# Optimization experiments

Hardware: AMD Instinct MI355X
Metric: run time of the kernel (lower is better)

Reference implementation:

```python
import jax, jax.numpy as jnp
import numpy as np

B, S, C = 16, 1024, 8
V, D, E, H, R = 50257, 512, 8, 512, 32
F, RT, CD, Q = 1024, 512, 64, 128
EPS = 1e-6


def _normalize(x):
    n = jnp.maximum(jnp.linalg.norm(x, axis=-1, keepdims=True), EPS)
    return x / n


def _fake_quantize(x):
    # F.normalize then straight-through int8 quant on the unit vector
    xn = _normalize(x)
    q = jnp.clip(jnp.round(xn * 127.0), -127.0, 127.0)
    return xn + jax.lax.stop_gradient(q / 127.0 - xn)


def setup_inputs() -> dict:
    key = jax.random.key(0)
    ks = iter(jax.random.split(key, 64))

    def w(shape, s=0.02):
        return (jax.random.normal(next(ks), shape, dtype=jnp.float32) * s)

    inp = {}
    inp['prefix_tokens'] = jax.random.randint(next(ks), (B, S), 0, V, dtype=jnp.int32)
    inp['chunk_inputs'] = jax.random.randint(next(ks), (B, C), 0, V, dtype=jnp.int32)
    inp['chunk_targets'] = jax.random.randint(next(ks), (B, C), 0, V, dtype=jnp.int32)
    inp['next_chunk_tokens'] = jax.random.randint(next(ks), (B, C), 0, V, dtype=jnp.int32)

    inp['emb'] = w((V, D))
    # stacked per-expert AffineExpert params
    inp['Wa'] = w((E, D, H)); inp['ba'] = jnp.zeros((E, H), jnp.float32)
    inp['Wg'] = w((E, D, R)); inp['bg'] = jnp.zeros((E, R), jnp.float32)
    inp['Wu'] = w((E, D, H)); inp['bu'] = jnp.zeros((E, H), jnp.float32)
    inp['u_mat'] = w((E, H, R)); inp['v_mat'] = w((E, H, R))
    inp['Wp'] = w((E, H, F)); inp['bp'] = jnp.zeros((E, F), jnp.float32)
    # gate MLP
    inp['Wg1'] = w((D, D)); inp['bg1'] = jnp.zeros((D,), jnp.float32)
    inp['Wg2'] = w((D, E)); inp['bg2'] = jnp.zeros((E,), jnp.float32)
    # query / target / key / code-expansion / write-code
    inp['Wq'] = w((F, Q)); inp['bq'] = jnp.zeros((Q,), jnp.float32)
    inp['Wt1'] = w((2 * D, RT)); inp['bt1'] = jnp.zeros((RT,), jnp.float32)
    inp['Wt2'] = w((RT, RT)); inp['bt2'] = jnp.zeros((RT,), jnp.float32)
    inp['Wk'] = w((RT, Q)); inp['bk'] = jnp.zeros((Q,), jnp.float32)
    inp['Web'] = w((CD, RT))  # expansion_basis (no bias)
    inp['Wwc'] = w((F, CD)); inp['bwc'] = jnp.zeros((CD,), jnp.float32)
    # ctx MLP
    inp['Wc1'] = w((2 * F, F)); inp['bc1'] = jnp.zeros((F,), jnp.float32)
    inp['Wc2'] = w((F, F)); inp['bc2'] = jnp.zeros((F,), jnp.float32)
    # chunk decoder
    inp['chunk_pos'] = w((C, F))
    inp['Wci'] = w((D + F, F)); inp['bci'] = jnp.zeros((F,), jnp.float32)
    inp['Wm1'] = w((F, F)); inp['bm1'] = jnp.zeros((F,), jnp.float32)
    inp['Wm2'] = w((F, F)); inp['bm2'] = jnp.zeros((F,), jnp.float32)
    inp['Wlm'] = w((F, V)); inp['blm'] = jnp.zeros((V,), jnp.float32)
    return inp


def _expert_scan(x, Wa, ba, Wg, bg, Wu, bu, u_mat, v_mat):
    # x: [B,S,D]; precompute all per-step projections as one big GEMM each,
    # leading axis = time for lax.scan. A,U: [S,E,B,H], G: [S,E,B,R]
    A = jax.nn.sigmoid(jnp.einsum('bsd,edh->sebh', x, Wa) + ba[None, :, None, :])
    G = jnp.einsum('bsd,edr->sebr', x, Wg) + bg[None, :, None, :]
    U = jnp.einsum('bsd,edh->sebh', x, Wu) + bu[None, :, None, :]

    def step(state, inp):  # state: [E,B,H]
        a, g, u = inp
        low = jnp.einsum('ebh,ehr->ebr', state, v_mat) * g
        state = a * state + u + jnp.einsum('ebr,ehr->ebh', low, u_mat)
        return state, None

    state0 = jnp.zeros((E, B, H), x.dtype)
    state, _ = jax.lax.scan(step, state0, (A, G, U))
    return state  # [E,B,H]


def reference(prefix_tokens, chunk_inputs, chunk_targets, next_chunk_tokens,
              emb, Wa, ba, Wg, bg, Wu, bu, u_mat, v_mat, Wp, bp,
              Wg1, bg1, Wg2, bg2, Wq, bq, Wt1, bt1, Wt2, bt2, Wk, bk,
              Web, Wwc, bwc, Wc1, bc1, Wc2, bc2,
              chunk_pos, Wci, bci, Wm1, bm1, Wm2, bm2, Wlm, blm):
    # ---- encode_prefix ----
    prefix_emb = emb[prefix_tokens]                       # [B,S,D]
    summary = prefix_emb.mean(axis=1)                     # [B,D]
    gate_probs = jax.nn.softmax(jax.nn.silu(summary @ Wg1 + bg1) @ Wg2 + bg2, axis=-1)  # [B,E]
    states = _expert_scan(prefix_emb, Wa, ba, Wg, bg, Wu, bu, u_mat, v_mat)             # [E,B,H]
    proj = jnp.einsum('ebh,ehf->ebf', states, Wp) + bp[:, None, :]                       # [E,B,F]
    fused = jnp.einsum('ebf,be->bf', proj, gate_probs)    # [B,F]

    # ---- query / target / key ----
    q_st = _fake_quantize(fused @ Wq + bq)                # [B,Q]
    chunk_emb = emb[chunk_targets].mean(axis=1)           # [B,D]
    next_emb = emb[next_chunk_tokens].mean(axis=1)        # [B,D]
    t_in = jnp.concatenate([chunk_emb, next_emb], axis=-1)
    target_state = _normalize(jax.nn.silu(t_in @ Wt1 + bt1) @ Wt2 + bt2)  # [B,RT]
    target_k_st = _fake_quantize(target_state @ Wk + bk)  # [B,Q]

    # ---- read_context (bank=None path -> zero read) ----
    zero_read = jnp.zeros_like(fused)
    c_in = jnp.concatenate([fused, zero_read], axis=-1)
    ctx = jax.nn.silu(c_in @ Wc1 + bc1) @ Wc2 + bc2       # [B,F]

    # ---- write_from_ctx ----
    write_codes = ctx @ Wwc + bwc                         # [B,CD]
    write_state = _normalize(write_codes @ Web)           # [B,RT]
    write_k_st = _fake_quantize(write_state @ Wk + bk)    # [B,Q]

    # ---- decode_chunk ----
    tok = emb[chunk_inputs]                               # [B,C,D]
    ctx_rep = jnp.broadcast_to(ctx[:, None, :], (B, C, F))
    hidden = jnp.concatenate([tok, ctx_rep], axis=-1) @ Wci + bci + chunk_pos[None]  # [B,C,F]
    hidden = jax.nn.silu(hidden @ Wm1 + bm1) @ Wm2 + bm2
    logits = hidden @ Wlm + blm                           # [B,C,V]

    # ---- losses ----
    logp = jax.nn.log_softmax(logits, axis=-1)
    token_loss = -jnp.take_along_axis(logp, chunk_targets[..., None], axis=-1)[..., 0]
    loss_nll = token_loss.mean()
    sim = (q_st @ target_k_st.T) / jnp.sqrt(jnp.float32(Q))  # [B,B]
    return logits, loss_nll, sim, write_k_st
```

## Files before the change

### kernel.cpp

```cpp
#include <hip/hip_runtime.h>
#include <math.h>

constexpr int BB = 16;
constexpr int SS = 1024;
constexpr int CC = 8;
constexpr int VV = 50257;
constexpr int DD = 512;
constexpr int EE = 8;
constexpr int HH = 512;
constexpr int RR = 32;
constexpr int FF = 1024;
constexpr int RTd = 512;
constexpr int CDd = 64;
constexpr int QQ = 128;
constexpr int SCH = 128;

typedef short bf16x8 __attribute__((ext_vector_type(8)));
typedef float f32x4 __attribute__((ext_vector_type(4)));

__device__ __forceinline__ float sigm(float x){ return 1.0f/(1.0f+expf(-x)); }

__device__ __forceinline__ unsigned short f2bf(float f){
  unsigned int u = __float_as_uint(f);
  u += 0x7fff + ((u>>16)&1);
  return (unsigned short)(u>>16);
}
__device__ __forceinline__ float bf2f(unsigned short h){
  return __uint_as_float(((unsigned int)h)<<16);
}

__device__ __forceinline__ void gload16(unsigned short* l, const unsigned short* g){
  __builtin_amdgcn_global_load_lds(
      (const __attribute__((address_space(1))) unsigned int*)(g),
      (__attribute__((address_space(3))) unsigned int*)(l), 16, 0, 0);
}

__global__ __launch_bounds__(256) void gather_pack(const int* __restrict__ toks,
    const float* __restrict__ emb, unsigned short* __restrict__ xp){
  int id = blockIdx.x*256 + threadIdx.x;
  int b = id >> 17;
  int rem = id & 131071;
  int c = rem >> 14;
  int rem2 = rem & 16383;
  int kc = rem2 >> 10;
  int pb = rem2 & 1023;
  int row = pb >> 3, q = pb & 7;
  int v = q ^ (row & 7);
  int kq = v >> 1, h = v & 1;
  int tok = toks[b*SS + c*128 + row];
  const float* src = emb + (size_t)tok*DD + kc*32 + kq*8;
  unsigned short o[8];
  #pragma unroll
  for (int j=0;j<8;j++){
    float f = src[j];
    unsigned short hi = f2bf(f);
    o[j] = h ? f2bf(f - bf2f(hi)) : hi;
  }
  ushort4* dst = (ushort4*)(xp + (size_t)id*8);
  dst[0] = make_ushort4(o[0],o[1],o[2],o[3]);
  dst[1] = make_ushort4(o[4],o[5],o[6],o[7]);
}

__global__ __launch_bounds__(512) void colsum_part(const int* __restrict__ toks,
    const float* __restrict__ emb, float* __restrict__ part){
  int b = blockIdx.y, j = blockIdx.x, d = threadIdx.x;
  float s = 0.f;
  for (int k=0;k<64;k++){
    int tok = toks[b*SS + j*64 + k];
    s += emb[(size_t)tok*DD + d];
  }
  part[(b*16 + j)*DD + d] = s;
}
__global__ __launch_bounds__(512) void colsum_final(const float* __restrict__ part,
                                                    float* __restrict__ summary){
  int b = blockIdx.x, d = threadIdx.x;
  float s = 0.f;
  for (int j=0;j<16;j++) s += part[(b*16 + j)*DD + d];
  summary[b*DD + d] = s * (1.0f/1024.0f);
}

__global__ __launch_bounds__(128) void gate_h1(const float* __restrict__ summary,
                                               const float* __restrict__ Wg1,
                                               const float* __restrict__ bg1,
                                               float* __restrict__ h1){
  int t = threadIdx.x; int j = blockIdx.x*128 + t;
  __shared__ float sm[16*512];
  for (int idx=t; idx<8192; idx+=128) sm[idx] = summary[idx];
  __syncthreads();
  float acc[16] = {0};
  for (int d=0; d<DD; d++){
    float w = Wg1[d*DD + j];
    #pragma unroll
    for (int b2=0;b2<16;b2++) acc[b2] += sm[b2*DD + d]*w;
  }
  #pragma unroll
  for (int b2=0;b2<16;b2++){ float v = acc[b2] + bg1[j]; h1[b2*DD + j] = v*sigm(v); }
}
__global__ __launch_bounds__(128) void gate_probs_k(const float* __restrict__ h1,
                                                    const float* __restrict__ Wg2,
                                                    const float* __restrict__ bg2,
                                                    float* __restrict__ gate){
  int t = threadIdx.x;
  int b = t>>3, e = t&7;
  float acc = bg2[e];
  for (int d=0; d<DD; d++) acc += h1[b*DD + d]*Wg2[d*EE + e];
  __shared__ float lg[16][8];
  lg[b][e] = acc;
  __syncthreads();
  if (e==0){
    float m = -3.4e38f;
    for (int i=0;i<8;i++) m = fmaxf(m, lg[b][i]);
    float s = 0.f; float ex[8];
    for (int i=0;i<8;i++){ ex[i] = expf(lg[b][i]-m); s += ex[i]; }
    for (int i=0;i<8;i++) gate[b*EE + i] = ex[i]/s;
  }
}

__global__ __launch_bounds__(256) void convT_pack_au(const float* __restrict__ Wa,
    const float* __restrict__ Wu, unsigned short* __restrict__ WPackAU){
  const int bid = blockIdx.x;
  const int e = bid >> 5;
  const int au = (bid >> 4) & 1;
  const int kc = bid & 15;
  const float* W = (au ? Wu : Wa) + (size_t)e*DD*HH + (size_t)kc*32*HH;
  __shared__ float tw[32][513];
  const int t = threadIdx.x;
  for (int i=0;i<64;i++){
    int id = t + i*256;
    int c = id & 511, k = id >> 9;
    tw[k][c] = W[(size_t)k*HH + c];
  }
  __syncthreads();
  for (int i=0;i<16;i++){
    int slot = t + i*256;
    int wq = slot >> 10, rem = slot & 1023;
    int cf = rem >> 7, hl = (rem >> 6) & 1, lane = rem & 63;
    int col = wq*128 + cf*16 + (lane & 15);
    int kb = lane >> 4;
    unsigned short o[8];
    #pragma unroll
    for (int j=0;j<8;j++){
      float f = tw[kb*8 + j][col];
      unsigned short hi = f2bf(f);
      o[j] = hl ? f2bf(f - bf2f(hi)) : hi;
    }
    size_t dst = (size_t)(e*2+au)*524288 + (size_t)(wq*16 + kc)*8192
               + (size_t)(cf*2 + hl)*512 + lane*8;
    *(ushort4*)&WPackAU[dst]   = make_ushort4(o[0],o[1],o[2],o[3]);
    *(ushort4*)&WPackAU[dst+4] = make_ushort4(o[4],o[5],o[6],o[7]);
  }
}
__global__ __launch_bounds__(256) void convT_pack_g(const float* __restrict__ Wge,
    unsigned short* __restrict__ WPG){
  const int kc = blockIdx.x;
  __shared__ float tg[32][257];
  const int t = threadIdx.x;
  for (int i=0;i<32;i++){
    int id = t + i*256;
    int r = id & 31, k = (id >> 5) & 31, e = id >> 10;
    tg[k][e*32 + r] = Wge[((size_t)e*DD + kc*32 + k)*RR + r];
  }
  __syncthreads();
  for (int i=0;i<8;i++){
    int slot = t + i*256;
    int w = slot >> 8, rem = slot & 255;
    int cf = rem >> 7, hl = (rem >> 6) & 1, lane = rem & 63;
    int gcol = w*32 + cf*16 + (lane & 15);
    int kb = lane >> 4;
    unsigned short o[8];
    #pragma unroll
    for (int j=0;j<8;j++){
      float f = tg[kb*8 + j][gcol];
      unsigned short hi = f2bf(f);
      o[j] = hl ? f2bf(f - bf2f(hi)) : hi;
    }
    size_t dst = (((size_t)(w*16 + kc)*2 + cf)*2 + hl)*512 + lane*8;
    *(ushort4*)&WPG[dst]   = make_ushort4(o[0],o[1],o[2],o[3]);
    *(ushort4*)&WPG[dst+4] = make_ushort4(o[4],o[5],o[6],o[7]);
  }
}

__global__ __launch_bounds__(512, 2) void aug_scan(
    const unsigned short* __restrict__ xp,
    const unsigned short* __restrict__ WPackAU, const unsigned short* __restrict__ WPG,
    const float* __restrict__ ba, const float* __restrict__ bu, const float* __restrict__ bge,
    float* __restrict__ Aw, float* __restrict__ Uw, float* __restrict__ Gw,
    const float* __restrict__ Ar, const float* __restrict__ Ur, const float* __restrict__ Gr,
    const float* __restrict__ v_mat, const float* __restrict__ u_mat,
    float* __restrict__ states,
    int s0, int do_aug, int do_scan)
{
  __shared__ __align__(16) unsigned short lds[65536];
  const int t = threadIdx.x;
  const int xcd  = blockIdx.x & 7;
  const int slot = blockIdx.x >> 3;

  if (slot < 16){
    if (!do_scan) return;
    const int e = xcd;
    const int b = slot;
    const int r = t & 31, grp = t >> 5;
    float* stf   = (float*)lds;
    float* partf = (float*)lds + 1024;
    float* lowf  = (float*)lds + 1312;
    float vreg[32];
    #pragma unroll
    for (int i=0;i<32;i++) vreg[i] = v_mat[((size_t)e*HH + grp*32 + i)*RR + r];
    float ureg[32];
    {
      const float4* up = (const float4*)(u_mat + ((size_t)e*HH + t)*RR);
      #pragma unroll
      for (int j=0;j<8;j++){
        float4 v4 = up[j];
        ureg[j*4+0]=v4.x; ureg[j*4+1]=v4.y; ureg[j*4+2]=v4.z; ureg[j*4+3]=v4.w;
      }
    }
    const size_t sbase = ((size_t)e*BB + b)*HH + t;
    const size_t abase = ((size_t)e*BB + b)*SCH*HH + t;
    const size_t gbase = ((size_t)e*BB + b)*SCH*RR + r;
    float streg = states[sbase];
    stf[t] = streg;
    float a0 = Ar[abase], u0 = Ur[abase];
    float g0 = (t < 32) ? Gr[gbase] : 0.f;
    float a1 = Ar[abase + HH], u1 = Ur[abase + HH];
    float g1 = (t < 32) ? Gr[gbase + RR] : 0.f;
    __syncthreads();
    int cur = 0;
    for (int s=0; s<SCH; s++){
      float a2 = 0.f, u2 = 0.f, g2 = 0.f;
      if (s+2 < SCH){
        a2 = Ar[abase + (size_t)(s+2)*HH];
        u2 = Ur[abase + (size_t)(s+2)*HH];
        if (t < 32) g2 = Gr[gbase + (size_t)(s+2)*RR];
      }
      {
        const float* sp = &stf[cur*512 + grp*32];
        float p0=0.f,p1=0.f,p2=0.f,p3=0.f;
        #pragma unroll
        for (int i=0;i<8;i++){
          p0 += sp[i]    *vreg[i];
          p1 += sp[8+i]  *vreg[8+i];
          p2 += sp[16+i] *vreg[16+i];
          p3 += sp[24+i] *vreg[24+i];
        }
        float p = (p0+p1)+(p2+p3);
        p += __shfl_xor(p, 32, 64);
        if ((t & 32) == 0) partf[r*9 + (grp>>1)] = p;
      }
      __syncthreads();
      if (t < 32){
        float ss2 = 0.f;
        #pragma unroll
        for (int j=0;j<8;j++) ss2 += partf[t*9 + j];
        lowf[t] = ss2 * g0;
      }
      __syncthreads();
      {
        float q0=0.f,q1=0.f,q2=0.f,q3=0.f;
        #pragma unroll
        for (int i=0;i<8;i++){
          q0 += lowf[i]   *ureg[i];
          q1 += lowf[8+i] *ureg[8+i];
          q2 += lowf[16+i]*ureg[16+i];
          q3 += lowf[24+i]*ureg[24+i];
        }
        streg = a0*streg + u0 + ((q0+q1)+(q2+q3));
      }
      stf[(cur^1)*512 + t] = streg;
      cur ^= 1;
      a0=a1; u0=u1; g0=g1; a1=a2; u1=u2; g1=g2;
      __syncthreads();
    }
    states[sbase] = streg;
    return;
  }

  if (!do_aug) return;
  const int lane = t & 63, wv = t >> 6;
  const int cl15 = lane & 15;
  const int kb = lane >> 4;
  const int cix = s0 >> 7;

  if (slot < 48){
    const int e = xcd;
    const int idx = slot - 16;
    const int b = idx & 15;
    const int r0 = (idx >> 4) * 64;
    const unsigned short* xpc = xp + (((size_t)(b*8 + cix)) << 17);
    const int au = wv >> 2, wq = wv & 3;
    const unsigned short* wb = WPackAU + (size_t)(e*2+au)*524288 + (size_t)wq*16*8192;

    {
      const int kc = wv;
      const unsigned short* src = xpc + kc*8192 + r0*64;
      unsigned short* dst = lds + kc*4096;
      #pragma unroll
      for (int i=0;i<8;i++)
        gload16(dst + i*512, src + (size_t)(i*64 + lane)*8);
    }
    __syncthreads();
    {
      const int kc = 8 + wv;
      const unsigned short* src = xpc + kc*8192 + r0*64;
      unsigned short* dst = lds + kc*4096;
      #pragma unroll
      for (int i=0;i<8;i++)
        gload16(dst + i*512, src + (size_t)(i*64 + lane)*8);
    }

    f32x4 acc[4][8] = {};
    for (int half=0; half<2; half++){
      if (half) __syncthreads();
      for (int kc = half*8; kc < half*8 + 8; kc++){
        bf16x8 ah[4], al[4];
        #pragma unroll
        for (int rf=0; rf<4; rf++){
          const int rloc = rf*16 + cl15;
          const int qh = (kb*2) ^ (rloc & 7);
          ah[rf] = *(const bf16x8*)&lds[kc*4096 + rloc*64 + qh*8];
          al[rf] = *(const bf16x8*)&lds[kc*4096 + rloc*64 + (qh^1)*8];
        }
        #pragma unroll
        for (int cf=0; cf<8; cf++){
          const unsigned short* fp = wb + ((size_t)kc*8 + cf)*1024 + lane*8;
          bf16x8 bh = *(const bf16x8*)fp;
          bf16x8 bl = *(const bf16x8*)(fp + 512);
          #pragma unroll
          for (int rf=0; rf<4; rf++){
            acc[rf][cf] = __builtin_amdgcn_mfma_f32_16x16x32_bf16(ah[rf], bh, acc[rf][cf], 0,0,0);
            acc[rf][cf] = __builtin_amdgcn_mfma_f32_16x16x32_bf16(ah[rf], bl, acc[rf][cf], 0,0,0);
            acc[rf][cf] = __builtin_amdgcn_mfma_f32_16x16x32_bf16(al[rf], bh, acc[rf][cf], 0,0,0);
          }
        }
      }
    }
    const float* bias = au ? bu : ba;
    float* dst = (au ? Uw : Aw) + ((size_t)(e*BB + b)*SCH + r0)*HH;
    #pragma unroll
    for (int rf=0; rf<4; rf++){
      #pragma unroll
      for (int cf=0; cf<8; cf++){
        const int col = wq*128 + cf*16 + cl15;
        const float bv = bias[e*HH + col];
        #pragma unroll
        for (int i=0;i<4;i++){
          const int rloc = rf*16 + (lane>>4)*4 + i;
          float v = acc[rf][cf][i] + bv;
          if (!au) v = sigm(v);
          dst[(size_t)rloc*HH + col] = v;
        }
      }
    }
  } else {
    const int idx2 = slot - 48;
    const int b = (xcd << 1) | (idx2 & 1);
    const int r0 = (idx2 >> 1) * 32;
    const unsigned short* xpc = xp + (((size_t)(b*8 + cix)) << 17);
    {
      const int kc = wv;
      const unsigned short* src = xpc + kc*8192 + r0*64;
      unsigned short* dst = lds + kc*2048;
      #pragma unroll
      for (int i=0;i<4;i++)
        gload16(dst + i*512, src + (size_t)(i*64 + lane)*8);
    }
    __syncthreads();
    {
      const int kc = 8 + wv;
      const unsigned short* src = xpc + kc*8192 + r0*64;
      unsigned short* dst = lds + kc*2048;
      #pragma unroll
      for (int i=0;i<4;i++)
        gload16(dst + i*512, src + (size_t)(i*64 + lane)*8);
    }
    f32x4 acc[2][2] = {};
    const unsigned short* wb = WPG + (size_t)wv*32768;
    for (int half=0; half<2; half++){
      if (half) __syncthreads();
      for (int kc = half*8; kc < half*8 + 8; kc++){
        bf16x8 ah[2], al[2];
        #pragma unroll
        for (int rf=0; rf<2; rf++){
          const int rloc = rf*16 + cl15;
          const int qh = (kb*2) ^ (rloc & 7);
          ah[rf] = *(const bf16x8*)&lds[kc*2048 + rloc*64 + qh*8];
          al[rf] = *(const bf16x8*)&lds[kc*2048 + rloc*64 + (qh^1)*8];
        }
        #pragma unroll
        for (int cf=0; cf<2; cf++){
          const unsigned short* fp = wb + ((size_t)kc*2 + cf)*1024 + lane*8;
          bf16x8 bh = *(const bf16x8*)fp;
          bf16x8 bl = *(const bf16x8*)(fp + 512);
          #pragma unroll
          for (int rf=0; rf<2; rf++){
            acc[rf][cf] = __builtin_amdgcn_mfma_f32_16x16x32_bf16(ah[rf], bh, acc[rf][cf], 0,0,0);
            acc[rf][cf] = __builtin_amdgcn_mfma_f32_16x16x32_bf16(ah[rf], bl, acc[rf][cf], 0,0,0);
            acc[rf][cf] = __builtin_amdgcn_mfma_f32_16x16x32_bf16(al[rf], bh, acc[rf][cf], 0,0,0);
          }
        }
      }
    }
    #pragma unroll
    for (int rf=0; rf<2; rf++){
      #pragma unroll
      for (int cf=0; cf<2; cf++){
        const int gcol = wv*32 + cf*16 + cl15;
        const int ee = gcol >> 5, r = gcol & 31;
        const float bv = bge[ee*RR + r];
        #pragma unroll
        for (int i=0;i<4;i++){
          const int rloc = rf*16 + (lane>>4)*4 + i;
          Gw[((size_t)(ee*BB + b)*SCH + r0 + rloc)*RR + r] = acc[rf][cf][i] + bv;
        }
      }
    }
  }
}

__global__ __launch_bounds__(128) void proj_partial(const float* __restrict__ states,
    const float* __restrict__ Wp, const float* __restrict__ gate, float* __restrict__ pf){
  int fc = blockIdx.x, e = blockIdx.y, t = threadIdx.x;
  __shared__ float stl[16*512];
  for (int idx=t; idx<8192; idx+=128) stl[idx] = states[(size_t)e*8192 + idx];
  __syncthreads();
  int f = fc*128 + t;
  float acc[16] = {0};
  for (int h=0; h<HH; h++){
    float w = Wp[((size_t)e*HH + h)*FF + f];
    #pragma unroll
    for (int b2=0;b2<16;b2++) acc[b2] += stl[b2*HH + h]*w;
  }
  #pragma unroll
  for (int b2=0;b2<16;b2++) pf[((size_t)(e*16 + b2))*FF + f] = gate[b2*EE + e]*acc[b2];
}
__global__ __launch_bounds__(256) void fuse_reduce(const float* __restrict__ pf,
    const float* __restrict__ gate, const float* __restrict__ bp, float* __restrict__ fused){
  int idx = blockIdx.x*256 + threadIdx.x;
  int b = idx >> 10, f = idx & 1023;
  float s = 0.f;
  #pragma unroll
  for (int e=0;e<8;e++) s += pf[((size_t)(e*16 + b))*FF + f] + gate[b*EE + e]*bp[e*FF + f];
  fused[idx] = s;
}

__global__ __launch_bounds__(128) void fq_linear(const float* __restrict__ in, int Kin,
    const float* __restrict__ W, const float* __restrict__ bias, float* __restrict__ out){
  int b = blockIdx.x, t = threadIdx.x;
  __shared__ float xin[1024];
  __shared__ float red[2];
  for (int k=t;k<Kin;k+=128) xin[k] = in[(size_t)b*Kin + k];
  __syncthreads();
  float acc = bias[t];
  for (int k=0;k<Kin;k++) acc += xin[k]*W[k*QQ + t];
  float ss = acc*acc;
  #pragma unroll
  for (int off=32; off; off>>=1) ss += __shfl_xor(ss, off, 64);
  if ((t&63)==0) red[t>>6] = ss;
  __syncthreads();
  float n = fmaxf(sqrtf(red[0]+red[1]), 1e-6f);
  float xn = acc / n;
  float q = fminf(fmaxf(rintf(xn*127.0f), -127.0f), 127.0f) * (1.0f/127.0f);
  out[b*QQ + t] = q;
}

__global__ __launch_bounds__(512) void chunk_means(const int* __restrict__ ct,
    const int* __restrict__ nct, const float* __restrict__ emb, float* __restrict__ tin){
  int b = blockIdx.x, d = threadIdx.x;
  float ce=0.f, ne=0.f;
  for (int c=0;c<CC;c++){
    ce += emb[(size_t)ct[b*CC+c]*DD + d];
    ne += emb[(size_t)nct[b*CC+c]*DD + d];
  }
  tin[b*1024 + d] = ce*0.125f;
  tin[b*1024 + 512 + d] = ne*0.125f;
}

__global__ __launch_bounds__(512) void target_state_kernel(const float* __restrict__ tin,
    const float* __restrict__ Wt1, const float* __restrict__ bt1,
    const float* __restrict__ Wt2, const float* __restrict__ bt2, float* __restrict__ outts){
  int b = blockIdx.x, t = threadIdx.x;
  __shared__ float xin[1024];
  __shared__ float h1[512];
  __shared__ float red[8];
  for (int k=t;k<1024;k+=512) xin[k] = tin[b*1024 + k];
  __syncthreads();
  float acc = bt1[t];
  for (int k=0;k<1024;k++) acc += xin[k]*Wt1[k*RTd + t];
  acc = acc*sigm(acc);
  h1[t] = acc;
  __syncthreads();
  float y = bt2[t];
  for (int k=0;k<512;k++) y += h1[k]*Wt2[k*RTd + t];
  float ss = y*y;
  #pragma unroll
  for (int off=32; off; off>>=1) ss += __shfl_xor(ss, off, 64);
  if ((t&63)==0) red[t>>6] = ss;
  __syncthreads();
  float tot = 0.f;
  #pragma unroll
  for (int i=0;i<8;i++) tot += red[i];
  float n = fmaxf(sqrtf(tot), 1e-6f);
  outts[b*RTd + t] = y/n;
}

__global__ __launch_bounds__(512) void write_state_kernel(const float* __restrict__ ctx,
    const float* __restrict__ Wwc, const float* __restrict__ bwc,
    const float* __restrict__ Web, float* __restrict__ wsn){
  int b = blockIdx.x, t = threadIdx.x;
  __shared__ float cx[1024];
  __shared__ float wc[64];
  __shared__ float red[8];
  for (int k=t;k<1024;k+=512) cx[k] = ctx[b*FF + k];
  __syncthreads();
  if (t < 64){
    float a = bwc[t];
    for (int k=0;k<1024;k++) a += cx[k]*Wwc[k*CDd + t];
    wc[t] = a;
  }
  __syncthreads();
  float y = 0.f;
  for (int k=0;k<64;k++) y += wc[k]*Web[k*RTd + t];
  float ss = y*y;
  #pragma unroll
  for (int off=32; off; off>>=1) ss += __shfl_xor(ss, off, 64);
  if ((t&63)==0) red[t>>6] = ss;
  __syncthreads();
  float tot = 0.f;
  #pragma unroll
  for (int i=0;i<8;i++) tot += red[i];
  float n = fmaxf(sqrtf(tot), 1e-6f);
  wsn[b*RTd + t] = y/n;
}

__global__ __launch_bounds__(256) void sim_kernel(const float* __restrict__ q,
    const float* __restrict__ k, float* __restrict__ out){
  int t = threadIdx.x;
  int i = t>>4, j = t&15;
  float s = 0.f;
  for (int c=0;c<QQ;c++) s += q[i*QQ + c]*k[j*QQ + c];
  out[t] = s / sqrtf(128.0f);
}

__global__ __launch_bounds__(256) void build_xcat(const int* __restrict__ ci,
    const float* __restrict__ emb, const float* __restrict__ ctx, float* __restrict__ xcat){
  int idx = blockIdx.x*256 + threadIdx.x;
  int row = idx / 1536, k = idx % 1536;
  float v = (k < DD) ? emb[(size_t)ci[row]*DD + k] : ctx[(row>>3)*FF + (k - DD)];
  xcat[idx] = v;
}

__global__ __launch_bounds__(256) void gemm_part(const float* __restrict__ X,
    const float* __restrict__ W, float* __restrict__ part,
    int K, int KS, int M){
  const int t = threadIdx.x;
  const int col = blockIdx.x*64 + (t & 63);
  const int r0 = blockIdx.y*16;
  const int ks = blockIdx.z;
  const int rg = t >> 6;
  const int kslice = K / KS;
  const int kbeg = ks*kslice;
  __shared__ float xs[16][65];
  float acc[4] = {};
  for (int k0=kbeg; k0<kbeg+kslice; k0+=64){
    #pragma unroll
    for (int i=0;i<4;i++){
      int id = t + i*256;
      int row = id >> 6, kk = id & 63;
      xs[row][kk] = X[(size_t)(r0+row)*K + k0 + kk];
    }
    __syncthreads();
    #pragma unroll 8
    for (int kk=0; kk<64; kk++){
      float w = W[(size_t)(k0+kk)*FF + col];
      #pragma unroll
      for (int i=0;i<4;i++) acc[i] += xs[rg*4+i][kk]*w;
    }
    __syncthreads();
  }
  #pragma unroll
  for (int i=0;i<4;i++)
    part[((size_t)ks*M + r0 + rg*4 + i)*FF + col] = acc[i];
}
__global__ __launch_bounds__(256) void gemm_combine(const float* __restrict__ part,
    const float* __restrict__ bias, const float* __restrict__ pos,
    float* __restrict__ outp, int KS, int M, int act){
  int idx = blockIdx.x*256 + threadIdx.x;
  int row = idx >> 10, col = idx & 1023;
  float v = bias[col];
  for (int k=0;k<KS;k++) v += part[(size_t)k*M*FF + idx];
  if (pos) v += pos[(row & 7)*FF + col];
  if (act) v = v*sigm(v);
  outp[idx] = v;
}

__global__ __launch_bounds__(256) void split_h(const float* __restrict__ hsrc,
    unsigned short* __restrict__ hh, unsigned short* __restrict__ hl){
  int idx = blockIdx.x*256 + threadIdx.x;
  float f = hsrc[idx];
  unsigned short h = f2bf(f);
  hh[idx] = h;
  hl[idx] = f2bf(f - bf2f(h));
}

__global__ __launch_bounds__(256) void logits_mfma(
    const unsigned short* __restrict__ hh, const unsigned short* __restrict__ hl,
    const float* __restrict__ Wlm, const float* __restrict__ blm,
    float* __restrict__ out){
  const int t = threadIdx.x;
  const int lane = t & 63, w = t >> 6;
  const int cb = blockIdx.x * 64;
  __shared__ __align__(16) unsigned short xsh[8*128*8];
  __shared__ __align__(16) unsigned short xsl[8*128*8];
  __shared__ __align__(16) unsigned short wsh[8*64*8];
  __shared__ __align__(16) unsigned short wsl[8*64*8];
  f32x4 acc[2][4] = {};
  for (int kc=0; kc<16; kc++){
    const int k0 = kc*64;
    #pragma unroll
    for (int i=0;i<4;i++){
      int id = t + i*256;
      int kq = id & 7, row = id >> 3;
      int pb = row*8 + (kq ^ (row&7));
      *(uint4*)&xsh[pb*8] = *(const uint4*)(hh + (size_t)row*FF + k0 + kq*8);
      *(uint4*)&xsl[pb*8] = *(const uint4*)(hl + (size_t)row*FF + k0 + kq*8);
    }
    #pragma unroll
    for (int i=0;i<2;i++){
      int id = t + i*256;
      int cc = id & 63, kq = id >> 6;
      int c = cb + cc; if (c >= VV) c = VV - 1;
      unsigned short h8[8], l8[8];
      #pragma unroll
      for (int j=0;j<8;j++){
        float f = Wlm[(size_t)(k0 + kq*8 + j)*VV + c];
        unsigned short h = f2bf(f);
        h8[j] = h;
        l8[j] = f2bf(f - bf2f(h));
      }
      int pb = kq*64 + cc;
      *(ushort4*)&wsh[pb*8]   = make_ushort4(h8[0],h8[1],h8[2],h8[3]);
      *(ushort4*)&wsh[pb*8+4] = make_ushort4(h8[4],h8[5],h8[6],h8[7]);
      *(ushort4*)&wsl[pb*8]   = make_ushort4(l8[0],l8[1],l8[2],l8[3]);
      *(ushort4*)&wsl[pb*8+4] = make_ushort4(l8[4],l8[5],l8[6],l8[7]);
    }
    __syncthreads();
    #pragma unroll
    for (int ks=0; ks<2; ks++){
      const int kq4 = ks*4 + (lane>>4);
      const int rr0 = w*32 + (lane&15);
      const int rr1 = rr0 + 16;
      bf16x8 ah0 = *(const bf16x8*)&xsh[(rr0*8 + (kq4^(rr0&7)))*8];
      bf16x8 ah1 = *(const bf16x8*)&xsh[(rr1*8 + (kq4^(rr1&7)))*8];
      bf16x8 al0 = *(const bf16x8*)&xsl[(rr0*8 + (kq4^(rr0&7)))*8];
      bf16x8 al1 = *(const bf16x8*)&xsl[(rr1*8 + (kq4^(rr1&7)))*8];
      #pragma unroll
      for (int cf=0; cf<4; cf++){
        const int cc = cf*16 + (lane&15);
        bf16x8 bh = *(const bf16x8*)&wsh[(kq4*64 + cc)*8];
        bf16x8 bl = *(const bf16x8*)&wsl[(kq4*64 + cc)*8];
        acc[0][cf] = __builtin_amdgcn_mfma_f32_16x16x32_bf16(ah0, bh, acc[0][cf], 0,0,0);
        acc[0][cf] = __builtin_amdgcn_mfma_f32_16x16x32_bf16(ah0, bl, acc[0][cf], 0,0,0);
        acc[0][cf] = __builtin_amdgcn_mfma_f32_16x16x32_bf16(al0, bh, acc[0][cf], 0,0,0);
        acc[1][cf] = __builtin_amdgcn_mfma_f32_16x16x32_bf16(ah1, bh, acc[1][cf], 0,0,0);
        acc[1][cf] = __builtin_amdgcn_mfma_f32_16x16x32_bf16(ah1, bl, acc[1][cf], 0,0,0);
        acc[1][cf] = __builtin_amdgcn_mfma_f32_16x16x32_bf16(al1, bh, acc[1][cf], 0,0,0);
      }
    }
    __syncthreads();
  }
  const int cl = lane & 15;
  const int r4 = (lane >> 4) * 4;
  #pragma unroll
  for (int rf=0; rf<2; rf++){
    #pragma unroll
    for (int cf=0; cf<4; cf++){
      int c = cb + cf*16 + cl;
      if (c >= VV) continue;
      float bb = blm[c];
      #pragma unroll
      for (int i=0;i<4;i++){
        int row = w*32 + rf*16 + r4 + i;
        out[(size_t)row*VV + c] = acc[rf][cf][i] + bb;
      }
    }
  }
}

__global__ __launch_bounds__(512) void softmax_nll(const float* __restrict__ logits,
    const int* __restrict__ tgt, float* __restrict__ tl){
  const int row = blockIdx.x;
  const float* p = logits + (size_t)row*VV;
  const int t = threadIdx.x;
  float m = -3.4e38f, s = 0.f;
  for (int c=t; c<VV; c+=512){
    float v = p[c];
    if (v > m){ s = s*expf(m - v) + 1.0f; m = v; }
    else s += expf(v - m);
  }
  #pragma unroll
  for (int off=32; off; off>>=1){
    float m2 = __shfl_xor(m, off, 64);
    float s2 = __shfl_xor(s, off, 64);
    float mn = fmaxf(m, m2);
    s = s*expf(m - mn) + s2*expf(m2 - mn);
    m = mn;
  }
  __shared__ float ms[8], ssh[8];
  if ((t&63)==0){ ms[t>>6] = m; ssh[t>>6] = s; }
  __syncthreads();
  if (t==0){
    float M = ms[0], S = ssh[0];
    for (int i=1;i<8;i++){
      float mn = fmaxf(M, ms[i]);
      S = S*expf(M-mn) + ssh[i]*expf(ms[i]-mn);
      M = mn;
    }
    tl[row] = M + logf(S) - p[tgt[row]];
  }
}
__global__ __launch_bounds__(128) void loss_reduce(const float* __restrict__ tl,
                                                   float* __restrict__ out){
  int t = threadIdx.x;
  float v = tl[t];
  #pragma unroll
  for (int off=32; off; off>>=1) v += __shfl_xor(v, off, 64);
  __shared__ float r2[2];
  if ((t&63)==0) r2[t>>6] = v;
  __syncthreads();
  if (t==0) out[0] = (r2[0]+r2[1]) * (1.0f/128.0f);
}

extern "C" void kernel_launch(void* const* d_in, const int* in_sizes, int n_in,
                              void* d_out, int out_size, void* d_ws, size_t ws_size,
                              hipStream_t stream){
  (void)in_sizes; (void)n_in; (void)out_size;
  const int*  prefix = (const int*)d_in[0];
  const int*  cinp   = (const int*)d_in[1];
  const int*  ctgt   = (const int*)d_in[2];
  const int*  nctk   = (const int*)d_in[3];
  const float* emb  = (const float*)d_in[4];
  const float* Wa   = (const float*)d_in[5];
  const float* ba   = (const float*)d_in[6];
  const float* Wge  = (const float*)d_in[7];
  const float* bge  = (const float*)d_in[8];
  const float* Wu   = (const float*)d_in[9];
  const float* bu   = (const float*)d_in[10];
  const float* u_mat= (const float*)d_in[11];
  const float* v_mat= (const float*)d_in[12];
  const float* Wp   = (const float*)d_in[13];
  const float* bp   = (const float*)d_in[14];
  const float* Wg1  = (const float*)d_in[15];
  const float* bg1  = (const float*)d_in[16];
  const float* Wg2  = (const float*)d_in[17];
  const float* bg2  = (const float*)d_in[18];
  const float* Wq   = (const float*)d_in[19];
  const float* bq   = (const float*)d_in[20];
  const float* Wt1  = (const float*)d_in[21];
  const float* bt1  = (const float*)d_in[22];
  const float* Wt2  = (const float*)d_in[23];
  const float* bt2  = (const float*)d_in[24];
  const float* Wk   = (const float*)d_in[25];
  const float* bk   = (const float*)d_in[26];
  const float* Web  = (const float*)d_in[27];
  const float* Wwc  = (const float*)d_in[28];
  const float* bwc  = (const float*)d_in[29];
  const float* Wc1  = (const float*)d_in[30];
  const float* bc1  = (const float*)d_in[31];
  const float* Wc2  = (const float*)d_in[32];
  const float* bc2  = (const float*)d_in[33];
  const float* cpos = (const float*)d_in[34];
  const float* Wci  = (const float*)d_in[35];
  const float* bci  = (const float*)d_in[36];
  const float* Wm1  = (const float*)d_in[37];
  const float* bm1  = (const float*)d_in[38];
  const float* Wm2  = (const float*)d_in[39];
  const float* bm2  = (const float*)d_in[40];
  const float* Wlm  = (const float*)d_in[41];
  const float* blm  = (const float*)d_in[42];

  float* ws = (float*)d_ws;
  size_t off = 0;
  unsigned short* xp = (unsigned short*)(ws + off); off += (size_t)BB*SS*DD;
  float* Abuf0  = ws + off; off += (size_t)SCH*EE*BB*HH;
  float* Ubuf0  = ws + off; off += (size_t)SCH*EE*BB*HH;
  float* Gbuf0  = ws + off; off += (size_t)SCH*EE*BB*RR;
  float* statesb= ws + off; off += (size_t)EE*BB*HH;
  float* partb  = ws + off; off += (size_t)BB*16*DD;
  float* summb  = ws + off; off += (size_t)BB*DD;
  float* h1b    = ws + off; off += (size_t)BB*DD;
  float* gateb  = ws + off; off += (size_t)BB*EE;
  float* pfb    = ws + off; off += (size_t)EE*BB*FF;
  float* fusedb = ws + off; off += (size_t)BB*FF;
  float* qstb   = ws + off; off += (size_t)BB*QQ;
  float* tinb   = ws + off; off += (size_t)BB*2*DD;
  float* tstb   = ws + off; off += (size_t)BB*RTd;
  float* tkb    = ws + off; off += (size_t)BB*QQ;
  float* ctxb   = ws + off; off += (size_t)BB*FF;
  float* hctxb  = ws + off; off += (size_t)BB*FF;
  float* wsnb   = ws + off; off += (size_t)BB*RTd;
  float* xcatb  = ws + off; off += (size_t)BB*CC*(DD+FF);
  float* hid1b  = ws + off; off += (size_t)BB*CC*FF;
  float* h2b    = ws + off; off += (size_t)BB*CC*FF;
  float* hidb   = ws + off; off += (size_t)BB*CC*FF;
  float* tlb    = ws + off; off += (size_t)BB*CC;
  float* ppart  = ws + off; off += (size_t)4*BB*CC*FF;
  unsigned short* WPackAU = (unsigned short*)(ws + off); off += (size_t)EE*DD*HH*2;
  unsigned short* WPG     = (unsigned short*)(ws + off); off += (size_t)EE*DD*RR;
  unsigned short* hhb  = (unsigned short*)(ws + off); off += (size_t)BB*CC*FF/2;
  unsigned short* hlb  = (unsigned short*)(ws + off); off += (size_t)BB*CC*FF/2;
  float* Abuf1  = ws + off; off += (size_t)SCH*EE*BB*HH;
  float* Ubuf1  = ws + off; off += (size_t)SCH*EE*BB*HH;
  float* Gbuf1  = ws + off; off += (size_t)SCH*EE*BB*RR;
  const bool fused = ws_size >= off * sizeof(float);

  float* out = (float*)d_out;
  const size_t LOGITS_OFF = 0;
  const size_t LOSS_OFF = (size_t)BB*CC*VV;
  const size_t SIM_OFF  = LOSS_OFF + 1;
  const size_t WK_OFF   = SIM_OFF + (size_t)BB*BB;

  convT_pack_au<<<256, 256, 0, stream>>>(Wa, Wu, WPackAU);
  convT_pack_g<<<16, 256, 0, stream>>>(Wge, WPG);

  gather_pack<<<8192, 256, 0, stream>>>(prefix, emb, xp);
  colsum_part<<<dim3(16,16), 512, 0, stream>>>(prefix, emb, partb);
  colsum_final<<<16, 512, 0, stream>>>(partb, summb);
  gate_h1<<<4, 128, 0, stream>>>(summb, Wg1, bg1, h1b);
  gate_probs_k<<<1, 128, 0, stream>>>(h1b, Wg2, bg2, gateb);

  hipMemsetAsync(statesb, 0, (size_t)EE*BB*HH*sizeof(float), stream);

  if (fused){
    for (int c=0; c<=8; c++){
      int da = (c<8) ? 1 : 0;
      int dscn = (c>=1) ? 1 : 0;
      float* Aw = (c&1) ? Abuf1 : Abuf0;
      float* Uw = (c&1) ? Ubuf1 : Ubuf0;
      float* Gw = (c&1) ? Gbuf1 : Gbuf0;
      const float* Ar = ((c-1)&1) ? Abuf1 : Abuf0;
      const float* Ur = ((c-1)&1) ? Ubuf1 : Ubuf0;
      const float* Gr = ((c-1)&1) ? Gbuf1 : Gbuf0;
      int grid = da ? 448 : 128;
      aug_scan<<<grid, 512, 0, stream>>>(xp, WPackAU, WPG, ba, bu, bge,
          Aw, Uw, Gw, Ar, Ur, Gr, v_mat, u_mat, statesb,
          c*SCH, da, dscn);
    }
  } else {
    for (int c=0; c<8; c++){
      aug_scan<<<448, 512, 0, stream>>>(xp, WPackAU, WPG, ba, bu, bge,
          Abuf0, Ubuf0, Gbuf0, Abuf0, Ubuf0, Gbuf0, v_mat, u_mat, statesb,
          c*SCH, 1, 0);
      aug_scan<<<128, 512, 0, stream>>>(xp, WPackAU, WPG, ba, bu, bge,
          Abuf0, Ubuf0, Gbuf0, Abuf0, Ubuf0, Gbuf0, v_mat, u_mat, statesb,
          c*SCH, 0, 1);
    }
  }

  proj_partial<<<dim3(8,8), 128, 0, stream>>>(statesb, Wp, gateb, pfb);
  fuse_reduce<<<64, 256, 0, stream>>>(pfb, gateb, bp, fusedb);

  fq_linear<<<16, 128, 0, stream>>>(fusedb, FF, Wq, bq, qstb);
  chunk_means<<<16, 512, 0, stream>>>(ctgt, nctk, emb, tinb);
  target_state_kernel<<<16, 512, 0, stream>>>(tinb, Wt1, bt1, Wt2, bt2, tstb);
  fq_linear<<<16, 128, 0, stream>>>(tstb, RTd, Wk, bk, tkb);

  gemm_part<<<dim3(16,1,4), 256, 0, stream>>>(fusedb, Wc1, ppart, FF, 4, 16);
  gemm_combine<<<64, 256, 0, stream>>>(ppart, bc1, nullptr, hctxb, 4, 16, 1);
  gemm_part<<<dim3(16,1,4), 256, 0, stream>>>(hctxb, Wc2, ppart, FF, 4, 16);
  gemm_combine<<<64, 256, 0, stream>>>(ppart, bc2, nullptr, ctxb, 4, 16, 0);

  write_state_kernel<<<16, 512, 0, stream>>>(ctxb, Wwc, bwc, Web, wsnb);
  fq_linear<<<16, 128, 0, stream>>>(wsnb, RTd, Wk, bk, out + WK_OFF);
  sim_kernel<<<1, 256, 0, stream>>>(qstb, tkb, out + SIM_OFF);

  build_xcat<<<768, 256, 0, stream>>>(cinp, emb, ctxb, xcatb);
  gemm_part<<<dim3(16,8,4), 256, 0, stream>>>(xcatb, Wci, ppart, DD+FF, 4, 128);
  gemm_combine<<<512, 256, 0, stream>>>(ppart, bci, cpos, hid1b, 4, 128, 0);
  gemm_part<<<dim3(16,8,4), 256, 0, stream>>>(hid1b, Wm1, ppart, FF, 4, 128);
  gemm_combine<<<512, 256, 0, stream>>>(ppart, bm1, nullptr, h2b, 4, 128, 1);
  gemm_part<<<dim3(16,8,4), 256, 0, stream>>>(h2b, Wm2, ppart, FF, 4, 128);
  gemm_combine<<<512, 256, 0, stream>>>(ppart, bm2, nullptr, hidb, 4, 128, 0);

  split_h<<<512, 256, 0, stream>>>(hidb, hhb, hlb);
  logits_mfma<<<(VV+63)/64, 256, 0, stream>>>(hhb, hlb, Wlm, blm, out + LOGITS_OFF);

  softmax_nll<<<BB*CC, 512, 0, stream>>>(out + LOGITS_OFF, ctgt, tlb);
  loss_reduce<<<1, 128, 0, stream>>>(tlb, out + LOSS_OFF);
}
```

Before: 1.699 ms.

## Double-buffer scan coefficients and aug x-tiles through LDS, shrinking LDS footprint

The scan branch now stages 8 steps of A/U/G coefficients at a time into LDS using async global-to-LDS loads, double-buffered, instead of per-thread register prefetch two steps ahead. The aug GEMM branch replaces its two-half full 16-chunk LDS load with a 4-stage double-buffered pipeline of 4 k-chunks each. Together these cut the static LDS allocation from 128KB to 80KB, which may let more blocks share a CU. The cost is extra waitcnt and barrier points per stage, plus some extra LDS traffic in the latency-bound scan loop.

Measured after the change: 1.703 ms. About the same (+0.3%).

```diff
diff --git a/kernel.cpp b/kernel.cpp
--- a/kernel.cpp
+++ b/kernel.cpp
@@ -190,19 +190,24 @@
     float* __restrict__ states,
     int s0, int do_aug, int do_scan)
 {
-  __shared__ __align__(16) unsigned short lds[65536];
+  __shared__ __align__(16) unsigned short lds[40960];
   const int t = threadIdx.x;
   const int xcd  = blockIdx.x & 7;
   const int slot = blockIdx.x >> 3;
+  const int lane = t & 63, wv = t >> 6;
 
   if (slot < 16){
     if (!do_scan) return;
     const int e = xcd;
     const int b = slot;
     const int r = t & 31, grp = t >> 5;
-    float* stf   = (float*)lds;
-    float* partf = (float*)lds + 1024;
-    float* lowf  = (float*)lds + 1312;
+    float* f     = (float*)lds;
+    float* stf   = f;
+    float* partf = f + 1024;
+    float* lowf  = f + 1312;
+    float* bufG  = f + 1536;
+    float* bufA  = f + 2048;
+    float* bufU  = f + 10240;
     float vreg[32];
     #pragma unroll
     for (int i=0;i<32;i++) vreg[i] = v_mat[((size_t)e*HH + grp*32 + i)*RR + r];
@@ -215,68 +220,80 @@
         ureg[j*4+0]=v4.x; ureg[j*4+1]=v4.y; ureg[j*4+2]=v4.z; ureg[j*4+3]=v4.w;
       }
     }
-    const size_t sbase = ((size_t)e*BB + b)*HH + t;
-    const size_t abase = ((size_t)e*BB + b)*SCH*HH + t;
-    const size_t gbase = ((size_t)e*BB + b)*SCH*RR + r;
+    const size_t sbase  = ((size_t)e*BB + b)*HH + t;
+    const size_t abase0 = ((size_t)e*BB + b)*SCH*HH;
+    const size_t gbase0 = ((size_t)e*BB + b)*SCH*RR;
+
+#define STAGE_S(BUF, BT) { \
+    const float* As_ = Ar + abase0 + (size_t)(BT)*8*HH + wv*512; \
+    const float* Us_ = Ur + abase0 + (size_t)(BT)*8*HH + wv*512; \
+    float* Ad_ = bufA + (BUF)*4096 + wv*512; \
+    float* Ud_ = bufU + (BUF)*4096 + wv*512; \
+    gload16((unsigned short*)Ad_,       (const unsigned short*)(As_ + lane*4)); \
+    gload16((unsigned short*)(Ad_+256), (const unsigned short*)(As_ + 256 + lane*4)); \
+    gload16((unsigned short*)Ud_,       (const unsigned short*)(Us_ + lane*4)); \
+    gload16((unsigned short*)(Ud_+256), (const unsigned short*)(Us_ + 256 + lane*4)); \
+    if (wv == 0) gload16((unsigned short*)(bufG + (BUF)*256), \
+                         (const unsigned short*)(Gr + gbase0 + (size_t)(BT)*256 + lane*4)); }
+
     float streg = states[sbase];
     stf[t] = streg;
-    float a0 = Ar[abase], u0 = Ur[abase];
-    float g0 = (t < 32) ? Gr[gbase] : 0.f;
-    float a1 = Ar[abase + HH], u1 = Ur[abase + HH];
-    float g1 = (t < 32) ? Gr[gbase + RR] : 0.f;
+    STAGE_S(0, 0)
+    asm volatile("s_waitcnt vmcnt(0)" ::: "memory");
     __syncthreads();
-    int cur = 0;
-    for (int s=0; s<SCH; s++){
-      float a2 = 0.f, u2 = 0.f, g2 = 0.f;
-      if (s+2 < SCH){
-        a2 = Ar[abase + (size_t)(s+2)*HH];
-        u2 = Ur[abase + (size_t)(s+2)*HH];
-        if (t < 32) g2 = Gr[gbase + (size_t)(s+2)*RR];
+    int cur = 0, pc = 0;
+    for (int bt=0; bt<16; bt++){
+      if (bt < 15) STAGE_S(cur^1, bt+1)
+      for (int s8=0; s8<8; s8++){
+        float a = bufA[cur*4096 + s8*512 + t];
+        float u = bufU[cur*4096 + s8*512 + t];
+        {
+          const float* sp = &stf[pc*512 + grp*32];
+          float p0=0.f,p1=0.f,p2=0.f,p3=0.f;
+          #pragma unroll
+          for (int i=0;i<8;i++){
+            p0 += sp[i]    *vreg[i];
+            p1 += sp[8+i]  *vreg[8+i];
+            p2 += sp[16+i] *vreg[16+i];
+            p3 += sp[24+i] *vreg[24+i];
+          }
+          float p = (p0+p1)+(p2+p3);
+          p += __shfl_xor(p, 32, 64);
+          if ((t & 32) == 0) partf[r*9 + (grp>>1)] = p;
+        }
+        __syncthreads();
+        if (t < 32){
+          float ss2 = 0.f;
+          #pragma unroll
+          for (int j=0;j<8;j++) ss2 += partf[t*9 + j];
+          lowf[t] = ss2 * bufG[cur*256 + s8*32 + t];
+        }
+        __syncthreads();
+        {
+          float q0=0.f,q1=0.f,q2=0.f,q3=0.f;
+          #pragma unroll
+          for (int i=0;i<8;i++){
+            q0 += lowf[i]   *ureg[i];
+            q1 += lowf[8+i] *ureg[8+i];
+            q2 += lowf[16+i]*ureg[16+i];
+            q3 += lowf[24+i]*ureg[24+i];
+          }
+          streg = a*streg + u + ((q0+q1)+(q2+q3));
+        }
+        stf[(pc^1)*512 + t] = streg;
+        pc ^= 1;
+        __syncthreads();
       }
-      {
-        const float* sp = &stf[cur*512 + grp*32];
-        float p0=0.f,p1=0.f,p2=0.f,p3=0.f;
-        #pragma unroll
-        for (int i=0;i<8;i++){
-          p0 += sp[i]    *vreg[i];
-          p1 += sp[8+i]  *vreg[8+i];
-          p2 += sp[16+i] *vreg[16+i];
-          p3 += sp[24+i] *vreg[24+i];
-        }
-        float p = (p0+p1)+(p2+p3);
-        p += __shfl_xor(p, 32, 64);
-        if ((t & 32) == 0) partf[r*9 + (grp>>1)] = p;
-      }
+      asm volatile("s_waitcnt vmcnt(0)" ::: "memory");
       __syncthreads();
-      if (t < 32){
-        float ss2 = 0.f;
-        #pragma unroll
-        for (int j=0;j<8;j++) ss2 += partf[t*9 + j];
-        lowf[t] = ss2 * g0;
-      }
-      __syncthreads();
-      {
-        float q0=0.f,q1=0.f,q2=0.f,q3=0.f;
-        #pragma unroll
-        for (int i=0;i<8;i++){
-          q0 += lowf[i]   *ureg[i];
-          q1 += lowf[8+i] *ureg[8+i];
-          q2 += lowf[16+i]*ureg[16+i];
-          q3 += lowf[24+i]*ureg[24+i];
-        }
-        streg = a0*streg + u0 + ((q0+q1)+(q2+q3));
-      }
-      stf[(cur^1)*512 + t] = streg;
       cur ^= 1;
-      a0=a1; u0=u1; g0=g1; a1=a2; u1=u2; g1=g2;
-      __syncthreads();
-    }
+    }
+#undef STAGE_S
     states[sbase] = streg;
     return;
   }
 
   if (!do_aug) return;
-  const int lane = t & 63, wv = t >> 6;
   const int cl15 = lane & 15;
   const int kb = lane >> 4;
   const int cix = s0 >> 7;
@@ -289,36 +306,34 @@
     const unsigned short* xpc = xp + (((size_t)(b*8 + cix)) << 17);
     const int au = wv >> 2, wq = wv & 3;
     const unsigned short* wb = WPackAU + (size_t)(e*2+au)*524288 + (size_t)wq*16*8192;
-
-    {
-      const int kc = wv;
-      const unsigned short* src = xpc + kc*8192 + r0*64;
-      unsigned short* dst = lds + kc*4096;
-      #pragma unroll
-      for (int i=0;i<8;i++)
-        gload16(dst + i*512, src + (size_t)(i*64 + lane)*8);
-    }
-    __syncthreads();
-    {
-      const int kc = 8 + wv;
-      const unsigned short* src = xpc + kc*8192 + r0*64;
-      unsigned short* dst = lds + kc*4096;
-      #pragma unroll
-      for (int i=0;i<8;i++)
-        gload16(dst + i*512, src + (size_t)(i*64 + lane)*8);
-    }
+    const int kcl_s = wv >> 1;
+    const int halfr = wv & 1;
+
+#define STAGE_Q(BUF, Q) { \
+    const int kcq_ = (Q)*4 + kcl_s; \
+    const unsigned short* src_ = xpc + kcq_*8192 + r0*64 + halfr*2048; \
+    unsigned short* dst_ = lds + (BUF)*16384 + kcl_s*4096 + halfr*2048; \
+    _Pragma("unroll") \
+    for (int i_=0;i_<4;i_++) gload16(dst_ + i_*512, src_ + (size_t)(i_*64 + lane)*8); }
+
+    STAGE_Q(0, 0)
+    asm volatile("s_waitcnt vmcnt(0)" ::: "memory");
+    __builtin_amdgcn_s_barrier();
 
     f32x4 acc[4][8] = {};
-    for (int half=0; half<2; half++){
-      if (half) __syncthreads();
-      for (int kc = half*8; kc < half*8 + 8; kc++){
+    int cur = 0;
+    for (int q=0; q<4; q++){
+      if (q < 3) STAGE_Q(cur^1, q+1)
+      for (int kc2=0; kc2<4; kc2++){
+        const int kc = q*4 + kc2;
+        const unsigned short* xb = lds + cur*16384 + kc2*4096;
         bf16x8 ah[4], al[4];
         #pragma unroll
         for (int rf=0; rf<4; rf++){
           const int rloc = rf*16 + cl15;
           const int qh = (kb*2) ^ (rloc & 7);
-          ah[rf] = *(const bf16x8*)&lds[kc*4096 + rloc*64 + qh*8];
-          al[rf] = *(const bf16x8*)&lds[kc*4096 + rloc*64 + (qh^1)*8];
+          ah[rf] = *(const bf16x8*)&xb[rloc*64 + qh*8];
+          al[rf] = *(const bf16x8*)&xb[rloc*64 + (qh^1)*8];
         }
         #pragma unroll
         for (int cf=0; cf<8; cf++){
@@ -333,7 +348,11 @@
           }
         }
       }
-    }
+      asm volatile("s_waitcnt vmcnt(0)" ::: "memory");
+      __builtin_amdgcn_s_barrier();
+      cur ^= 1;
+    }
+#undef STAGE_Q
     const float* bias = au ? bu : ba;
     float* dst = (au ? Uw : Aw) + ((size_t)(e*BB + b)*SCH + r0)*HH;
     #pragma unroll
```
